# Kernel optimization log

Measured on AMD Instinct MI355X. Metric: run time of the kernel, lower is better.

Reference implementation:

```python
import jax, jax.numpy as jnp
from jax import lax
import numpy as np

NUM_CH, LSTM_SIZE, NUM_CLS, SEQ_LEN, NUM_PROPS = 128, 512, 40, 256, 1024

def setup_inputs() -> dict:
    key = jax.random.key(0)
    ks = jax.random.split(key, 16)
    s = 0.05
    H, C = LSTM_SIZE, NUM_CH
    return {
        "data": jax.random.normal(ks[0], (NUM_PROPS, SEQ_LEN, C), jnp.float32),
        "labels": jax.random.randint(ks[1], (NUM_PROPS, 2), 0, NUM_CLS).astype(jnp.int32),
        "proposals": jax.random.uniform(ks[2], (NUM_PROPS, 2), jnp.float32),
        # layer 0 LSTM params (PyTorch gate order i,f,g,o; b = b_ih + b_hh)
        "W_ih_0": jax.random.normal(ks[3], (4 * H, C), jnp.float32) * s,
        "W_hh_0": jax.random.normal(ks[4], (4 * H, H), jnp.float32) * s,
        "b_0": jax.random.normal(ks[5], (4 * H,), jnp.float32) * s,
        # layer 1 LSTM params
        "W_ih_1": jax.random.normal(ks[6], (4 * H, H), jnp.float32) * s,
        "W_hh_1": jax.random.normal(ks[7], (4 * H, H), jnp.float32) * s,
        "b_1": jax.random.normal(ks[8], (4 * H,), jnp.float32) * s,
        # heads
        "W_cls": jax.random.normal(ks[9], (NUM_CLS, H), jnp.float32) * s,
        "b_cls": jnp.zeros((NUM_CLS,), jnp.float32),
        "W_bbox": jax.random.normal(ks[10], (2, H), jnp.float32) * s,
        "b_bbox": jnp.zeros((2,), jnp.float32),
    }

def _lstm_layer(x_tnc, W_ih, W_hh, b):
    # x_tnc: [T, N, C_in]; returns hidden sequence [T, N, H]
    T, N, _ = x_tnc.shape
    H = W_hh.shape[1]
    xg = jnp.einsum('tnc,gc->tng', x_tnc, W_ih) + b  # precompute input projections
    def step(carry, gx):
        h, c = carry
        g = gx + h @ W_hh.T
        i, f, gg, o = jnp.split(g, 4, axis=-1)
        i, f, o = jax.nn.sigmoid(i), jax.nn.sigmoid(f), jax.nn.sigmoid(o)
        c = f * c + i * jnp.tanh(gg)
        h = o * jnp.tanh(c)
        return (h, c), h
    h0 = jnp.zeros((N, H), x_tnc.dtype)
    _, hs = lax.scan(step, (h0, h0), xg)
    return hs

def _forward(data, labels, proposals,
             W_ih_0, W_hh_0, b_0, W_ih_1, W_hh_1, b_1,
             W_cls, b_cls, W_bbox, b_bbox):
    x = jnp.transpose(data, (1, 0, 2))  # [T, N, C]
    x = _lstm_layer(x, W_ih_0, W_hh_0, b_0)
    hs = _lstm_layer(x, W_ih_1, W_hh_1, b_1)
    base_feat = hs[-1]                   # last timestep, [N, H]
    cls_feat = base_feat @ W_cls.T + b_cls
    bbox_feat = base_feat @ W_bbox.T + b_bbox
    # train branch: cross-entropy / loss_div, smooth_l1 * 10
    lbl = labels[:, 0]
    logp = jax.nn.log_softmax(cls_feat, axis=-1)
    cls_loss = -jnp.mean(jnp.take_along_axis(logp, lbl[:, None], axis=1))
    cls_idx = jnp.argmax(cls_feat, axis=1)
    loss_div = 1.0 + jnp.sum((cls_idx == lbl).astype(cls_feat.dtype))
    cls_loss = cls_loss / lax.stop_gradient(loss_div)
    target = proposals / SEQ_LEN
    diff = jnp.abs(bbox_feat - target)
    sl1 = jnp.where(diff < 1.0, 0.5 * diff * diff, diff - 0.5)
    bbox_loss = jnp.mean(sl1) * 10.0
    return jnp.stack([cls_loss, bbox_loss])

def reference(data, labels, proposals,
              W_ih_0, W_hh_0, b_0, W_ih_1, W_hh_1, b_1,
              W_cls, b_cls, W_bbox, b_bbox):
    return _forward(data, labels, proposals,
                    W_ih_0, W_hh_0, b_0, W_ih_1, W_hh_1, b_1,
                    W_cls, b_cls, W_bbox, b_bbox)
```

## Files before the change

kernel.cpp:

```cpp
#include <hip/hip_runtime.h>

typedef unsigned short u16;
typedef __attribute__((ext_vector_type(8))) __bf16 bf16x8;
typedef __attribute__((ext_vector_type(4))) float f32x4;

#define T_SEQ 256
#define N_B   1024
#define C_IN  128
#define H_DIM 512
#define NCLS  40
#define NT0   20
#define NT1   32
#define HSLOT (16*1024*32)

union B8 { bf16x8 v; u16 s[8]; };

__device__ __forceinline__ u16 f32_to_bf16_rne(float x) {
    unsigned u = __float_as_uint(x);
    unsigned rounding = 0x7FFFu + ((u >> 16) & 1u);
    return (u16)((u + rounding) >> 16);
}
__device__ __forceinline__ float bf16_to_f32(u16 h) {
    return __uint_as_float(((unsigned)h) << 16);
}
__device__ __forceinline__ void split2(float x, u16& hi, u16& lo) {
    u16 h = f32_to_bf16_rne(x);
    float hf = bf16_to_f32(h);
    u16 l = f32_to_bf16_rne(x - hf);
    hi = h; lo = l;
}
__device__ __forceinline__ float fast_sigmoid(float x) {
    return 1.0f / (1.0f + __expf(-x));
}
__device__ __forceinline__ float fast_tanh(float x) {
    return 1.0f - 2.0f / (__expf(2.0f * x) + 1.0f);
}

__global__ void k_pack_w(const float* __restrict__ Wih, const float* __restrict__ Whh,
                         int KX, int NT, u16* __restrict__ hi, u16* __restrict__ lo) {
    size_t idx = (size_t)blockIdx.x * 256 + threadIdx.x;
    size_t total = (size_t)16 * NT * 128 * 32;
    if (idx >= total) return;
    int k = (int)(idx & 31);
    int r = (int)((idx >> 5) & 127);
    int rem = (int)(idx >> 12);
    int kt = rem % NT, ct = rem / NT;
    int gate = r & 3, jl = r >> 2;
    int srow = (gate << 9) + (ct << 5) + jl;
    int kg = (kt << 5) + k;
    float v = (kg < KX) ? Wih[(size_t)srow * KX + kg] : Whh[(size_t)srow * H_DIM + (kg - KX)];
    u16 h, l; split2(v, h, l);
    hi[idx] = h; lo[idx] = l;
}

__device__ __forceinline__ void lstm_tile_body(
    int local_blk,
    const float* __restrict__ Xf32,
    const u16* __restrict__ xAhi, const u16* __restrict__ xAlo, int nxt,
    const u16* __restrict__ hAhi, const u16* __restrict__ hAlo,
    const u16* __restrict__ Whi, const u16* __restrict__ Wlo, int NT,
    const float* __restrict__ bias, float* __restrict__ cbuf,
    u16* __restrict__ oHhi, u16* __restrict__ oHlo, float* __restrict__ oF32,
    char* lds, float* biasT)
{
    int ct = ((blockIdx.x & 7) << 1) | ((local_blk >> 6) & 1);
    int rt = (local_blk >> 3) & 7;
    int n0 = rt << 7;

    int tid  = threadIdx.x;
    int w    = tid >> 6;
    int l    = tid & 63;
    int quad = l >> 4;
    int lr   = l & 15;
    int wr   = (w & 1) << 6;
    int wc   = (w >> 1) << 5;

    if (tid < 128)
        biasT[tid] = bias[((tid & 3) << 9) + (ct << 5) + (tid >> 2)];

    const size_t wbase = ((size_t)(ct * NT)) << 12;
    bf16x8 sa_h, sa_l, sb_h, sb_l;

    auto load_stage = [&](int kt) {
        size_t wo = wbase + ((size_t)kt << 12) + ((size_t)tid << 3);
        sb_h = *(const bf16x8*)(Whi + wo);
        sb_l = *(const bf16x8*)(Wlo + wo);
        if (Xf32 != nullptr && kt < nxt) {
            int row = tid >> 2, seg = tid & 3;
            const float* p = Xf32 + (size_t)(n0 + row) * 32768 + (kt << 5) + (seg << 3);
            f32x4 x0 = *(const f32x4*)p;
            f32x4 x1 = *(const f32x4*)(p + 4);
            B8 hh, ll;
            #pragma unroll
            for (int e = 0; e < 4; e++) { u16 a, b; split2(x0[e], a, b); hh.s[e] = a; ll.s[e] = b; }
            #pragma unroll
            for (int e = 0; e < 4; e++) { u16 a, b; split2(x1[e], a, b); hh.s[4 + e] = a; ll.s[4 + e] = b; }
            sa_h = hh.v; sa_l = ll.v;
        } else {
            const u16 *ph, *pl; int kk;
            if (kt < nxt) { ph = xAhi; pl = xAlo; kk = kt; }
            else          { ph = hAhi; pl = hAlo; kk = kt - nxt; }
            size_t ao = (((size_t)kk * 1024 + n0) << 5) + ((size_t)tid << 3);
            sa_h = *(const bf16x8*)(ph + ao);
            sa_l = *(const bf16x8*)(pl + ao);
        }
    };
    auto write_stage = [&](char* buf) {
        *(bf16x8*)(buf + (tid << 4))         = sa_h;
        *(bf16x8*)(buf + 8192 + (tid << 4))  = sa_l;
        *(bf16x8*)(buf + 16384 + (tid << 4)) = sb_h;
        *(bf16x8*)(buf + 24576 + (tid << 4)) = sb_l;
    };

    f32x4 acc[4][2];
    #pragma unroll
    for (int i = 0; i < 4; i++)
        #pragma unroll
        for (int j = 0; j < 2; j++)
            acc[i][j] = (f32x4){0.f, 0.f, 0.f, 0.f};

    load_stage(0);
    write_stage(lds);
    __syncthreads();

    for (int tt = 0; tt < NT; tt++) {
        char* cur = lds + ((tt & 1) << 15);
        if (tt + 1 < NT) load_stage(tt + 1);

        bf16x8 ah[4], al[4], bh[2], bl[2];
        #pragma unroll
        for (int i = 0; i < 4; i++) {
            int ro = (wr + (i << 4) + lr) << 6;
            ah[i] = *(const bf16x8*)(cur + ro + (quad << 4));
            al[i] = *(const bf16x8*)(cur + 8192 + ro + (quad << 4));
        }
        #pragma unroll
        for (int j = 0; j < 2; j++) {
            int ro = (wc + (j << 4) + lr) << 6;
            bh[j] = *(const bf16x8*)(cur + 16384 + ro + (quad << 4));
            bl[j] = *(const bf16x8*)(cur + 24576 + ro + (quad << 4));
        }
        #pragma unroll
        for (int i = 0; i < 4; i++)
            #pragma unroll
            for (int j = 0; j < 2; j++) {
                acc[i][j] = __builtin_amdgcn_mfma_f32_16x16x32_bf16(ah[i], bh[j], acc[i][j], 0, 0, 0);
                acc[i][j] = __builtin_amdgcn_mfma_f32_16x16x32_bf16(al[i], bh[j], acc[i][j], 0, 0, 0);
                acc[i][j] = __builtin_amdgcn_mfma_f32_16x16x32_bf16(ah[i], bl[j], acc[i][j], 0, 0, 0);
            }

        if (tt + 1 < NT) write_stage(lds + (((tt + 1) & 1) << 15));
        __syncthreads();
    }

    float* Gs = (float*)lds;
    #pragma unroll
    for (int i = 0; i < 4; i++)
        #pragma unroll
        for (int j2 = 0; j2 < 2; j2++)
            #pragma unroll
            for (int r = 0; r < 4; r++)
                Gs[(wr + (i << 4) + (quad << 2) + r) * 128 + wc + (j2 << 4) + lr] = acc[i][j2][r];
    __syncthreads();

    int jl = tid & 31;
    int rbase = tid >> 5;
    #pragma unroll
    for (int it = 0; it < 8; it++) {
        int row = rbase + (it << 4);
        f32x4 gv = *(const f32x4*)(Gs + row * 128 + (jl << 2));
        float gi = gv[0] + biasT[(jl << 2) + 0];
        float gf = gv[1] + biasT[(jl << 2) + 1];
        float gg = gv[2] + biasT[(jl << 2) + 2];
        float go = gv[3] + biasT[(jl << 2) + 3];
        float si = fast_sigmoid(gi);
        float sf = fast_sigmoid(gf);
        float so = fast_sigmoid(go);
        int n = n0 + row;
        int cidx = (n << 9) + (ct << 5) + jl;
        float cn = sf * cbuf[cidx] + si * fast_tanh(gg);
        cbuf[cidx] = cn;
        float h = so * fast_tanh(cn);
        u16 hh2, hl2; split2(h, hh2, hl2);
        size_t ho = (((size_t)ct * 1024 + n) << 5) + jl;
        oHhi[ho] = hh2; oHlo[ho] = hl2;
        if (oF32) oF32[cidx] = h;
    }
}

__global__ __launch_bounds__(512) void k_lstm_pair(
    int t, const float* __restrict__ data,
    const u16* __restrict__ W0hi, const u16* __restrict__ W0lo,
    const u16* __restrict__ W1hi, const u16* __restrict__ W1lo,
    const float* __restrict__ b0, const float* __restrict__ b1,
    u16* __restrict__ h0hi, u16* __restrict__ h0lo,
    u16* __restrict__ h1hi, u16* __restrict__ h1lo,
    float* __restrict__ c0, float* __restrict__ c1,
    float* __restrict__ bfeat)
{
    __shared__ __align__(16) char lds[84096];
    __shared__ float biasT[128];
    int local_blk = blockIdx.x & 127;

    if (blockIdx.x < 128) {
        if (t == 0) return;
        int s = t - 1;
        const u16* xh = h0hi + (size_t)(s & 1) * HSLOT;
        const u16* xl = h0lo + (size_t)(s & 1) * HSLOT;
        const u16* hh = h1hi + (size_t)((s - 1) & 1) * HSLOT;
        const u16* hl = h1lo + (size_t)((s - 1) & 1) * HSLOT;
        u16* oh = h1hi + (size_t)(s & 1) * HSLOT;
        u16* ol = h1lo + (size_t)(s & 1) * HSLOT;
        lstm_tile_body(local_blk, nullptr, xh, xl, 16, hh, hl,
                       W1hi, W1lo, NT1, b1, c1, oh, ol,
                       (s == T_SEQ - 1) ? bfeat : nullptr, lds, biasT);
    } else {
        if (t >= T_SEQ) return;
        const u16* hh = h0hi + (size_t)((t - 1) & 1) * HSLOT;
        const u16* hl = h0lo + (size_t)((t - 1) & 1) * HSLOT;
        u16* oh = h0hi + (size_t)(t & 1) * HSLOT;
        u16* ol = h0lo + (size_t)(t & 1) * HSLOT;
        lstm_tile_body(local_blk, data + (size_t)t * C_IN, nullptr, nullptr, 4,
                       hh, hl, W0hi, W0lo, NT0, b0, c0, oh, ol,
                       nullptr, lds, biasT);
    }
}

__global__ __launch_bounds__(64) void k_head(
    const float* __restrict__ hfeat, const float* __restrict__ Wcls, const float* __restrict__ bcls,
    const float* __restrict__ Wbb, const float* __restrict__ bbb,
    const int* __restrict__ labels, const float* __restrict__ props,
    float* __restrict__ accum)
{
    __shared__ float hs[H_DIM];
    __shared__ float logits[NCLS];
    __shared__ float bb[2];
    int n = blockIdx.x, t = threadIdx.x;
    for (int k = t; k < H_DIM; k += 64) hs[k] = hfeat[((size_t)n << 9) + k];
    __syncthreads();
    if (t < NCLS) {
        float s = bcls[t];
        const float* w = Wcls + (size_t)t * H_DIM;
        for (int k = 0; k < H_DIM; k++) s += hs[k] * w[k];
        logits[t] = s;
    } else if (t < NCLS + 2) {
        int j = t - NCLS;
        float s = bbb[j];
        const float* w = Wbb + (size_t)j * H_DIM;
        for (int k = 0; k < H_DIM; k++) s += hs[k] * w[k];
        bb[j] = s;
    }
    __syncthreads();
    if (t == 0) {
        float m = logits[0]; int am = 0;
        for (int j = 1; j < NCLS; j++) if (logits[j] > m) { m = logits[j]; am = j; }
        float se = 0.f;
        for (int j = 0; j < NCLS; j++) se += expf(logits[j] - m);
        int lbl = labels[n * 2];
        float logp = logits[lbl] - m - logf(se);
        atomicAdd(&accum[0], -logp);
        if (am == lbl) atomicAdd(&accum[1], 1.0f);
        float s2 = 0.f;
        for (int j = 0; j < 2; j++) {
            float target = props[n * 2 + j] * (1.0f / 256.0f);
            float d = fabsf(bb[j] - target);
            s2 += (d < 1.f) ? 0.5f * d * d : d - 0.5f;
        }
        atomicAdd(&accum[2], s2);
    }
}

__global__ void k_final(const float* __restrict__ accum, float* __restrict__ out) {
    out[0] = (accum[0] * (1.0f / 1024.0f)) / (1.0f + accum[1]);
    out[1] = accum[2] * (10.0f / 2048.0f);
}

extern "C" void kernel_launch(void* const* d_in, const int* in_sizes, int n_in,
                              void* d_out, int out_size, void* d_ws, size_t ws_size,
                              hipStream_t stream) {
    const float* data  = (const float*)d_in[0];
    const int*   labels= (const int*)d_in[1];
    const float* props = (const float*)d_in[2];
    const float* Wih0  = (const float*)d_in[3];
    const float* Whh0  = (const float*)d_in[4];
    const float* b0    = (const float*)d_in[5];
    const float* Wih1  = (const float*)d_in[6];
    const float* Whh1  = (const float*)d_in[7];
    const float* b1    = (const float*)d_in[8];
    const float* Wcls  = (const float*)d_in[9];
    const float* bcls  = (const float*)d_in[10];
    const float* Wbb   = (const float*)d_in[11];
    const float* bbb   = (const float*)d_in[12];
    float* out = (float*)d_out;

    char* ws = (char*)d_ws;
    size_t off = 0;
    auto alloc = [&](size_t bytes) -> void* {
        void* p = ws + off;
        off = (off + bytes + 255) & ~(size_t)255;
        return p;
    };
    const size_t NH = (size_t)N_B * H_DIM;
    const size_t W0E = (size_t)16 * NT0 * 128 * 32;
    const size_t W1E = (size_t)16 * NT1 * 128 * 32;

    u16* W0hi = (u16*)alloc(W0E * 2);
    u16* W0lo = (u16*)alloc(W0E * 2);
    u16* W1hi = (u16*)alloc(W1E * 2);
    u16* W1lo = (u16*)alloc(W1E * 2);
    u16* h0hi = (u16*)alloc(2 * (size_t)HSLOT * 2);
    u16* h0lo = (u16*)alloc(2 * (size_t)HSLOT * 2);
    u16* h1hi = (u16*)alloc(2 * (size_t)HSLOT * 2);
    u16* h1lo = (u16*)alloc(2 * (size_t)HSLOT * 2);
    float* c0   = (float*)alloc(NH * 4);
    float* c1   = (float*)alloc(NH * 4);
    float* bfeat= (float*)alloc(NH * 4);
    float* accum= (float*)alloc(4 * 4);

    k_pack_w<<<(int)(W0E / 256), 256, 0, stream>>>(Wih0, Whh0, C_IN, NT0, W0hi, W0lo);
    k_pack_w<<<(int)(W1E / 256), 256, 0, stream>>>(Wih1, Whh1, H_DIM, NT1, W1hi, W1lo);

    (void)hipMemsetAsync(h0hi + HSLOT, 0, (size_t)HSLOT * 2, stream);
    (void)hipMemsetAsync(h0lo + HSLOT, 0, (size_t)HSLOT * 2, stream);
    (void)hipMemsetAsync(h1hi + HSLOT, 0, (size_t)HSLOT * 2, stream);
    (void)hipMemsetAsync(h1lo + HSLOT, 0, (size_t)HSLOT * 2, stream);
    (void)hipMemsetAsync(c0, 0, NH * 4, stream);
    (void)hipMemsetAsync(c1, 0, NH * 4, stream);
    (void)hipMemsetAsync(accum, 0, 16, stream);

    for (int t = 0; t <= T_SEQ; t++) {
        k_lstm_pair<<<256, 512, 0, stream>>>(
            t, data, W0hi, W0lo, W1hi, W1lo, b0, b1,
            h0hi, h0lo, h1hi, h1lo, c0, c1, bfeat);
    }

    k_head<<<N_B, 64, 0, stream>>>(bfeat, Wcls, bcls, Wbb, bbb, labels, props, accum);
    k_final<<<1, 1, 0, stream>>>(accum, out);
}
```

Baseline: 8.896 ms.

## Load MFMA fragments directly from global with register double-buffering, smaller tiles

Drops the LDS staging of A and B operands. Each wave now loads its own bf16 hi/lo fragments straight from global memory into two register sets that alternate across k-steps. Tiles shrink from 128x128 to 64x128 per block, with 128 threads per block and 512 blocks, so more blocks run per step. The aim is to cut LDS traffic and barriers in the recurrent step, at the cost of more redundant global/L2 loads and higher register pressure.

```diff
diff --git a/kernel.cpp b/kernel.cpp
--- a/kernel.cpp
+++ b/kernel.cpp
@@ -53,41 +53,25 @@
     hi[idx] = h; lo[idx] = l;
 }
 
-__device__ __forceinline__ void lstm_tile_body(
-    int local_blk,
+struct Frag16 { bf16x8 ah[4], al[4], bh[4], bl[4]; };
+
+__device__ __forceinline__ void load_frags(Frag16& F, int kt,
     const float* __restrict__ Xf32,
-    const u16* __restrict__ xAhi, const u16* __restrict__ xAlo, int nxt,
-    const u16* __restrict__ hAhi, const u16* __restrict__ hAlo,
-    const u16* __restrict__ Whi, const u16* __restrict__ Wlo, int NT,
-    const float* __restrict__ bias, float* __restrict__ cbuf,
-    u16* __restrict__ oHhi, u16* __restrict__ oHlo, float* __restrict__ oF32,
-    char* lds, float* biasT)
+    const u16* __restrict__ xhi, const u16* __restrict__ xlo, int nxt,
+    const u16* __restrict__ hhi, const u16* __restrict__ hlo,
+    const u16* __restrict__ Whi, const u16* __restrict__ Wlo,
+    int wbase, int n0, int wc, int quad, int lr)
 {
-    int ct = ((blockIdx.x & 7) << 1) | ((local_blk >> 6) & 1);
-    int rt = (local_blk >> 3) & 7;
-    int n0 = rt << 7;
-
-    int tid  = threadIdx.x;
-    int w    = tid >> 6;
-    int l    = tid & 63;
-    int quad = l >> 4;
-    int lr   = l & 15;
-    int wr   = (w & 1) << 6;
-    int wc   = (w >> 1) << 5;
-
-    if (tid < 128)
-        biasT[tid] = bias[((tid & 3) << 9) + (ct << 5) + (tid >> 2)];
-
-    const size_t wbase = ((size_t)(ct * NT)) << 12;
-    bf16x8 sa_h, sa_l, sb_h, sb_l;
-
-    auto load_stage = [&](int kt) {
-        size_t wo = wbase + ((size_t)kt << 12) + ((size_t)tid << 3);
-        sb_h = *(const bf16x8*)(Whi + wo);
-        sb_l = *(const bf16x8*)(Wlo + wo);
-        if (Xf32 != nullptr && kt < nxt) {
-            int row = tid >> 2, seg = tid & 3;
-            const float* p = Xf32 + (size_t)(n0 + row) * 32768 + (kt << 5) + (seg << 3);
+    #pragma unroll
+    for (int j = 0; j < 4; j++) {
+        size_t o = ((size_t)(wbase + kt) * 128 + wc + (j << 4) + lr) * 32 + (quad << 3);
+        F.bh[j] = *(const bf16x8*)(Whi + o);
+        F.bl[j] = *(const bf16x8*)(Wlo + o);
+    }
+    if (Xf32 != nullptr && kt < nxt) {
+        #pragma unroll
+        for (int i = 0; i < 4; i++) {
+            const float* p = Xf32 + (size_t)(n0 + (i << 4) + lr) * 32768 + (kt << 5) + (quad << 3);
             f32x4 x0 = *(const f32x4*)p;
             f32x4 x1 = *(const f32x4*)(p + 4);
             B8 hh, ll;
@@ -95,79 +79,91 @@
             for (int e = 0; e < 4; e++) { u16 a, b; split2(x0[e], a, b); hh.s[e] = a; ll.s[e] = b; }
             #pragma unroll
             for (int e = 0; e < 4; e++) { u16 a, b; split2(x1[e], a, b); hh.s[4 + e] = a; ll.s[4 + e] = b; }
-            sa_h = hh.v; sa_l = ll.v;
-        } else {
-            const u16 *ph, *pl; int kk;
-            if (kt < nxt) { ph = xAhi; pl = xAlo; kk = kt; }
-            else          { ph = hAhi; pl = hAlo; kk = kt - nxt; }
-            size_t ao = (((size_t)kk * 1024 + n0) << 5) + ((size_t)tid << 3);
-            sa_h = *(const bf16x8*)(ph + ao);
-            sa_l = *(const bf16x8*)(pl + ao);
+            F.ah[i] = hh.v; F.al[i] = ll.v;
         }
-    };
-    auto write_stage = [&](char* buf) {
-        *(bf16x8*)(buf + (tid << 4))         = sa_h;
-        *(bf16x8*)(buf + 8192 + (tid << 4))  = sa_l;
-        *(bf16x8*)(buf + 16384 + (tid << 4)) = sb_h;
-        *(bf16x8*)(buf + 24576 + (tid << 4)) = sb_l;
-    };
-
-    f32x4 acc[4][2];
+    } else {
+        const u16 *ph, *pl; int kk;
+        if (kt < nxt) { ph = xhi; pl = xlo; kk = kt; }
+        else          { ph = hhi; pl = hlo; kk = kt - nxt; }
+        #pragma unroll
+        for (int i = 0; i < 4; i++) {
+            size_t o = (((size_t)kk * 1024 + n0 + (i << 4) + lr) << 5) + (quad << 3);
+            F.ah[i] = *(const bf16x8*)(ph + o);
+            F.al[i] = *(const bf16x8*)(pl + o);
+        }
+    }
+}
+
+__device__ __forceinline__ void mfma48(const Frag16& F, f32x4 acc[4][4]) {
     #pragma unroll
     for (int i = 0; i < 4; i++)
         #pragma unroll
-        for (int j = 0; j < 2; j++)
+        for (int j = 0; j < 4; j++) {
+            acc[i][j] = __builtin_amdgcn_mfma_f32_16x16x32_bf16(F.ah[i], F.bh[j], acc[i][j], 0, 0, 0);
+            acc[i][j] = __builtin_amdgcn_mfma_f32_16x16x32_bf16(F.al[i], F.bh[j], acc[i][j], 0, 0, 0);
+            acc[i][j] = __builtin_amdgcn_mfma_f32_16x16x32_bf16(F.ah[i], F.bl[j], acc[i][j], 0, 0, 0);
+        }
+}
+
+__device__ __forceinline__ void lstm_tile_body(
+    int blk,
+    const float* __restrict__ Xf32,
+    const u16* __restrict__ xhi, const u16* __restrict__ xlo, int nxt,
+    const u16* __restrict__ hhi, const u16* __restrict__ hlo,
+    const u16* __restrict__ Whi, const u16* __restrict__ Wlo, int NT,
+    const float* __restrict__ bias, float* __restrict__ cbuf,
+    u16* __restrict__ oHhi, u16* __restrict__ oHlo, float* __restrict__ oF32,
+    float* Gs, float* biasT)
+{
+    int ct = ((blk & 7) << 1) | ((blk >> 3) & 1);
+    int rt = blk >> 4;
+    int n0 = rt << 6;
+
+    int tid  = threadIdx.x;
+    int w    = tid >> 6;
+    int l    = tid & 63;
+    int quad = l >> 4;
+    int lr   = l & 15;
+    int wc   = w << 6;
+
+    biasT[tid] = bias[((tid & 3) << 9) + (ct << 5) + (tid >> 2)];
+
+    int wbase = ct * NT;
+
+    f32x4 acc[4][4];
+    #pragma unroll
+    for (int i = 0; i < 4; i++)
+        #pragma unroll
+        for (int j = 0; j < 4; j++)
             acc[i][j] = (f32x4){0.f, 0.f, 0.f, 0.f};
 
-    load_stage(0);
-    write_stage(lds);
-    __syncthreads();
-
-    for (int tt = 0; tt < NT; tt++) {
-        char* cur = lds + ((tt & 1) << 15);
-        if (tt + 1 < NT) load_stage(tt + 1);
-
-        bf16x8 ah[4], al[4], bh[2], bl[2];
-        #pragma unroll
-        for (int i = 0; i < 4; i++) {
-            int ro = (wr + (i << 4) + lr) << 6;
-            ah[i] = *(const bf16x8*)(cur + ro + (quad << 4));
-            al[i] = *(const bf16x8*)(cur + 8192 + ro + (quad << 4));
-        }
-        #pragma unroll
-        for (int j = 0; j < 2; j++) {
-            int ro = (wc + (j << 4) + lr) << 6;
-            bh[j] = *(const bf16x8*)(cur + 16384 + ro + (quad << 4));
-            bl[j] = *(const bf16x8*)(cur + 24576 + ro + (quad << 4));
-        }
-        #pragma unroll
-        for (int i = 0; i < 4; i++)
-            #pragma unroll
-            for (int j = 0; j < 2; j++) {
-                acc[i][j] = __builtin_amdgcn_mfma_f32_16x16x32_bf16(ah[i], bh[j], acc[i][j], 0, 0, 0);
-                acc[i][j] = __builtin_amdgcn_mfma_f32_16x16x32_bf16(al[i], bh[j], acc[i][j], 0, 0, 0);
-                acc[i][j] = __builtin_amdgcn_mfma_f32_16x16x32_bf16(ah[i], bl[j], acc[i][j], 0, 0, 0);
-            }
-
-        if (tt + 1 < NT) write_stage(lds + (((tt + 1) & 1) << 15));
-        __syncthreads();
-    }
-
-    float* Gs = (float*)lds;
+    Frag16 Fa, Fb;
+    load_frags(Fa, 0, Xf32, xhi, xlo, nxt, hhi, hlo, Whi, Wlo, wbase, n0, wc, quad, lr);
+    int tt = 0;
+    for (; tt + 2 < NT; tt += 2) {
+        load_frags(Fb, tt + 1, Xf32, xhi, xlo, nxt, hhi, hlo, Whi, Wlo, wbase, n0, wc, quad, lr);
+        mfma48(Fa, acc);
+        load_frags(Fa, tt + 2, Xf32, xhi, xlo, nxt, hhi, hlo, Whi, Wlo, wbase, n0, wc, quad, lr);
+        mfma48(Fb, acc);
+    }
+    load_frags(Fb, NT - 1, Xf32, xhi, xlo, nxt, hhi, hlo, Whi, Wlo, wbase, n0, wc, quad, lr);
+    mfma48(Fa, acc);
+    mfma48(Fb, acc);
+
     #pragma unroll
     for (int i = 0; i < 4; i++)
         #pragma unroll
-        for (int j2 = 0; j2 < 2; j2++)
+        for (int j = 0; j < 4; j++)
             #pragma unroll
             for (int r = 0; r < 4; r++)
-                Gs[(wr + (i << 4) + (quad << 2) + r) * 128 + wc + (j2 << 4) + lr] = acc[i][j2][r];
+                Gs[((i << 4) + (quad << 2) + r) * 128 + wc + (j << 4) + lr] = acc[i][j][r];
     __syncthreads();
 
     int jl = tid & 31;
-    int rbase = tid >> 5;
-    #pragma unroll
-    for (int it = 0; it < 8; it++) {
-        int row = rbase + (it << 4);
+    int r0 = tid >> 5;
+    #pragma unroll
+    for (int it = 0; it < 16; it++) {
+        int row = r0 + (it << 2);
         f32x4 gv = *(const f32x4*)(Gs + row * 128 + (jl << 2));
         float gi = gv[0] + biasT[(jl << 2) + 0];
         float gf = gv[1] + biasT[(jl << 2) + 1];
@@ -188,7 +184,7 @@
     }
 }
 
-__global__ __launch_bounds__(512) void k_lstm_pair(
+__global__ __launch_bounds__(128) void k_lstm_pair(
     int t, const float* __restrict__ data,
     const u16* __restrict__ W0hi, const u16* __restrict__ W0lo,
     const u16* __restrict__ W1hi, const u16* __restrict__ W1lo,
@@ -198,11 +194,11 @@
     float* __restrict__ c0, float* __restrict__ c1,
     float* __restrict__ bfeat)
 {
-    __shared__ __align__(16) char lds[84096];
+    __shared__ __align__(16) float Gs[64 * 128];
     __shared__ float biasT[128];
-    int local_blk = blockIdx.x & 127;
-
-    if (blockIdx.x < 128) {
+    int blk = blockIdx.x & 255;
+
+    if (blockIdx.x < 256) {
         if (t == 0) return;
         int s = t - 1;
         const u16* xh = h0hi + (size_t)(s & 1) * HSLOT;
@@ -211,18 +207,18 @@
         const u16* hl = h1lo + (size_t)((s - 1) & 1) * HSLOT;
         u16* oh = h1hi + (size_t)(s & 1) * HSLOT;
         u16* ol = h1lo + (size_t)(s & 1) * HSLOT;
-        lstm_tile_body(local_blk, nullptr, xh, xl, 16, hh, hl,
+        lstm_tile_body(blk, nullptr, xh, xl, 16, hh, hl,
                        W1hi, W1lo, NT1, b1, c1, oh, ol,
-                       (s == T_SEQ - 1) ? bfeat : nullptr, lds, biasT);
+                       (s == T_SEQ - 1) ? bfeat : nullptr, Gs, biasT);
     } else {
         if (t >= T_SEQ) return;
         const u16* hh = h0hi + (size_t)((t - 1) & 1) * HSLOT;
         const u16* hl = h0lo + (size_t)((t - 1) & 1) * HSLOT;
         u16* oh = h0hi + (size_t)(t & 1) * HSLOT;
         u16* ol = h0lo + (size_t)(t & 1) * HSLOT;
-        lstm_tile_body(local_blk, data + (size_t)t * C_IN, nullptr, nullptr, 4,
+        lstm_tile_body(blk, data + (size_t)t * C_IN, nullptr, nullptr, 4,
                        hh, hl, W0hi, W0lo, NT0, b0, c0, oh, ol,
-                       nullptr, lds, biasT);
+                       nullptr, Gs, biasT);
     }
 }
 
@@ -329,7 +325,7 @@
     (void)hipMemsetAsync(accum, 0, 16, stream);
 
     for (int t = 0; t <= T_SEQ; t++) {
-        k_lstm_pair<<<256, 512, 0, stream>>>(
+        k_lstm_pair<<<512, 128, 0, stream>>>(
             t, data, W0hi, W0lo, W1hi, W1lo, b0, b1,
             h0hi, h0lo, h1hi, h1lo, c0, c1, bfeat);
     }
```

Measured after the change: 10.81 ms. +21.5%, slower.
